# Kernel tuning notes

Measured on AMD Instinct MI355X. Metric: run time of the kernel, lower is better.

Reference implementation:

```python
import jax, jax.numpy as jnp
import numpy as np

K_NEIGHBORS = 10
SINKHORN_REG = 0.1
SINKHORN_ITERS = 50
EPS = 1e-10


def _pairwise_dist(x):
    # Euclidean cdist; clamp avoids sqrt(0) NaN grads on the diagonal
    sq = jnp.sum(x * x, axis=1)
    d2 = sq[:, None] + sq[None, :] - 2.0 * (x @ x.T)
    return jnp.sqrt(jnp.maximum(d2, 1e-12))


def setup_inputs() -> dict:
    key = jax.random.key(0)
    k1, k2 = jax.random.split(key)
    n, d = 8192, 128
    return {
        "embeddings": jax.random.normal(k1, (n, d), dtype=jnp.float32),
        "reference_embeddings": jax.random.normal(k2, (n, d), dtype=jnp.float32),
    }


def reference(embeddings, reference_embeddings):
    k = min(K_NEIGHBORS, embeddings.shape[0] - 1)

    cur_d = _pairwise_dist(embeddings)              # [n, n]
    ref_d = _pairwise_dist(reference_embeddings)    # [n, n]

    # k+1 smallest (ascending), drop self-distance column
    cur_knn = jnp.sort(cur_d, axis=1)[:, 1:k + 1]   # [n, k]
    ref_knn = jnp.sort(ref_d, axis=1)[:, 1:k + 1]   # [n, k]

    a = cur_knn / (jnp.sum(cur_knn, axis=1, keepdims=True) + EPS)  # [n, k]
    b = ref_knn / (jnp.sum(ref_knn, axis=1, keepdims=True) + EPS)  # [n, k]

    idx = jnp.arange(k, dtype=jnp.float32)
    M = jnp.abs(idx[None, :] - idx[:, None]) / k    # [k, k] shared cost
    Kmat = jnp.exp(-M / SINKHORN_REG)               # [k, k]

    # Batched Sinkhorn across all n samples at once
    def step(u, _):
        v = b / (u @ Kmat + EPS)          # K.T @ u per sample (K symmetric; explicit form u @ K)
        u = a / (v @ Kmat.T + EPS)        # K @ v per sample
        return u, None

    u0 = jnp.ones_like(a)
    u, _ = jax.lax.scan(step, u0, None, length=SINKHORN_ITERS)
    v = b / (u @ Kmat + EPS)

    # sum_ij u_i K_ij M_ij v_j per sample, then mean over n
    per_sample = jnp.einsum('ni,ij,nj->n', u, Kmat * M, v)
    return jnp.mean(per_sample)
```

## Files before the change

kernel.cpp:

```cpp
#include <hip/hip_runtime.h>
#include <hip/hip_bf16.h>
#include <math.h>

#define N 8192
#define D 128
#define NELEM (N * D)
#define KNN 10
#define EPSF 1e-10f
#define RT 32
#define NSLICE 8
#define RH 1024
#define BIGF 3.0e38f

typedef unsigned short ushort_t;
typedef short bf16x8 __attribute__((ext_vector_type(8)));
typedef float f32x4 __attribute__((ext_vector_type(4)));

template <int L>
__device__ __forceinline__ void insM(float (&l)[L], float v) {
  #pragma unroll
  for (int q = L - 1; q >= 1; --q)
    l[q] = __builtin_amdgcn_fmed3f(l[q - 1], l[q], v);
  l[0] = fminf(l[0], v);
}

__global__ void prep_kernel(const float* __restrict__ xc,
                            const float* __restrict__ xr,
                            ushort_t* __restrict__ xb,
                            ushort_t* __restrict__ xa,
                            float* __restrict__ sq) {
  int wid  = (blockIdx.x * blockDim.x + threadIdx.x) >> 6;
  int lane = threadIdx.x & 63;
  if (wid >= 2 * N) return;
  const float* x = (wid < N) ? xc : xr;
  int row = (wid < N) ? wid : wid - N;
  float2 v = *reinterpret_cast<const float2*>(x + (size_t)row * D + lane * 2);
  float s = v.x * v.x + v.y * v.y;
  #pragma unroll
  for (int off = 32; off; off >>= 1) s += __shfl_xor(s, off, 64);
  if (lane == 0) sq[wid] = s;
  auto cvt = [](float f) -> unsigned int {
    unsigned int b = __float_as_uint(f);
    return (b + 0x7FFFu + ((b >> 16) & 1u)) >> 16;
  };
  unsigned int pb = cvt(v.x) | (cvt(v.y) << 16);
  unsigned int pa = cvt(-2.f * v.x) | (cvt(-2.f * v.y) << 16);
  *reinterpret_cast<unsigned int*>(xb + (size_t)wid * D + lane * 2) = pb;
  *reinterpret_cast<unsigned int*>(xa + (size_t)wid * D + lane * 2) = pa;
}

__global__ __launch_bounds__(256, 4) void knn_mfma(
    const ushort_t* __restrict__ xb,
    const ushort_t* __restrict__ xa,
    const float* __restrict__ sq,
    float* __restrict__ partial) {
  __shared__ __align__(16) ushort_t Abuf[2][RT * D];
  __shared__ __align__(16) float SQs[RH];

  const int bid = blockIdx.x;
  const int mat = bid >> 9;
  const int colblk = (bid >> 3) & 63;
  const int slice = bid & 7;
  const ushort_t* __restrict__ XB = xb + (size_t)mat * NELEM;
  const ushort_t* __restrict__ XA = xa + (size_t)mat * NELEM;
  const float* __restrict__ SQ = sq + mat * N;
  const int r0 = slice * RH;
  const int t = threadIdx.x;
  const int w = t >> 6, l = t & 63;
  const int c0w = colblk * 128 + w * 32;

  {
    const float* gs = SQ + r0 + w * 256 + l * 4;
    float* dsts = &SQs[w * 256];
    __builtin_amdgcn_global_load_lds(
        (const __attribute__((address_space(1))) void*)gs,
        (__attribute__((address_space(3))) void*)dsts, 16, 0, 0);
  }

  bf16x8 bfr[2][4];
  #pragma unroll
  for (int j = 0; j < 2; ++j) {
    const ushort_t* p = XB + (size_t)(c0w + j * 16 + (l & 15)) * D + (l >> 4) * 8;
    #pragma unroll
    for (int kk = 0; kk < 4; ++kk)
      bfr[j][kk] = *reinterpret_cast<const bf16x8*>(p + kk * 32);
  }

  float cand[2][KNN];
  #pragma unroll
  for (int j = 0; j < 2; ++j)
    #pragma unroll
    for (int q = 0; q < KNN; ++q) cand[j][q] = BIGF;

  auto stage = [&](int tt, int bb) {
    const ushort_t* rowg = XA + (size_t)(r0 + tt * RT) * D;
    #pragma unroll
    for (int h = 0; h < 2; ++h) {
      const int rg = 2 * w + h;
      const int kk = rg >> 1, ii = rg & 1;
      const int row = ii * 16 + (l & 15);
      const int ch  = kk * 4 + (l >> 4);
      const ushort_t* g = rowg + row * D + ch * 8;
      ushort_t* dst = &Abuf[bb][rg * 512];
      __builtin_amdgcn_global_load_lds(
          (const __attribute__((address_space(1))) void*)g,
          (__attribute__((address_space(3))) void*)dst, 16, 0, 0);
    }
  };

  stage(0, 0);
  asm volatile("s_waitcnt vmcnt(0)" ::: "memory");
  __syncthreads();

  for (int tt = 0; tt < RH / RT; ++tt) {
    const int cur = tt & 1;
    if (tt < RH / RT - 1) stage(tt + 1, cur ^ 1);

    f32x4 sqi[2];
    #pragma unroll
    for (int i = 0; i < 2; ++i)
      sqi[i] = *reinterpret_cast<const f32x4*>(
          &SQs[tt * RT + i * 16 + ((l >> 4) << 2)]);

    f32x4 acc[2][2];
    #pragma unroll
    for (int i = 0; i < 2; ++i)
      #pragma unroll
      for (int j = 0; j < 2; ++j) acc[i][j] = sqi[i];

    #pragma unroll
    for (int kk = 0; kk < 4; ++kk) {
      bf16x8 af[2];
      #pragma unroll
      for (int i = 0; i < 2; ++i)
        af[i] = *reinterpret_cast<const bf16x8*>(
            &Abuf[cur][(kk * 2 + i) * 512 + l * 8]);
      #pragma unroll
      for (int i = 0; i < 2; ++i)
        #pragma unroll
        for (int j = 0; j < 2; ++j)
          acc[i][j] = __builtin_amdgcn_mfma_f32_16x16x32_bf16(af[i], bfr[j][kk],
                                                              acc[i][j], 0, 0, 0);
    }

    const int rbase = r0 + tt * RT;
    const int idiff = c0w - rbase;
    if ((unsigned)(idiff + 31) < 63u) {
      #pragma unroll
      for (int i = 0; i < 2; ++i)
        #pragma unroll
        for (int j = 0; j < 2; ++j) {
          const int dd = idiff + j * 16 + (l & 15) - i * 16 - ((l >> 4) << 2);
          #pragma unroll
          for (int r = 0; r < 4; ++r)
            if (dd == r) acc[i][j][r] = BIGF;
        }
    }

    #pragma unroll
    for (int r = 0; r < 4; ++r)
      #pragma unroll
      for (int i = 0; i < 2; ++i)
        #pragma unroll
        for (int j = 0; j < 2; ++j)
          insM<KNN>(cand[j], acc[i][j][r]);

    asm volatile("s_waitcnt vmcnt(0)" ::: "memory");
    __syncthreads();
  }

  #pragma unroll
  for (int step = 16; step <= 32; step <<= 1)
    #pragma unroll
    for (int j = 0; j < 2; ++j)
      #pragma unroll
      for (int q = 0; q < KNN; ++q) {
        float o = __shfl_xor(cand[j][q], step, 64);
        insM<KNN>(cand[j], o);
      }

  if (l < 16) {
    #pragma unroll
    for (int j = 0; j < 2; ++j) {
      const int c = c0w + j * 16 + l;
      float* dst = partial + ((size_t)(mat * N + c) * NSLICE + slice) * KNN;
      #pragma unroll
      for (int q = 0; q < KNN; ++q) dst[q] = cand[j][q];
    }
  }
}

__global__ void sink_kernel(const float* __restrict__ partial,
                            const float* __restrict__ sq,
                            float* __restrict__ ps) {
  int s = blockIdx.x * blockDim.x + threadIdx.x;
  if (s >= N) return;
  constexpr float E1 = 0.36787944117144233f;

  float a[KNN], b[KNN];
  #pragma unroll
  for (int m = 0; m < 2; ++m) {
    float best[KNN];
    #pragma unroll
    for (int q = 0; q < KNN; ++q) best[q] = BIGF;
    const float* p = partial + (size_t)(m * N + s) * NSLICE * KNN;
    for (int c = 0; c < NSLICE * KNN; ++c) insM<KNN>(best, p[c]);
    const float sqc = sq[m * N + s];
    float* dst = m ? b : a;
    #pragma unroll
    for (int q = 0; q < KNN; ++q)
      dst[q] = sqrtf(fmaxf(best[q] + sqc, 1e-12f));
  }

  float suma = 0.f, sumb = 0.f;
  #pragma unroll
  for (int q = 0; q < KNN; ++q) { suma += a[q]; sumb += b[q]; }
  float rsa = __builtin_amdgcn_rcpf(suma + EPSF);
  float rsb = __builtin_amdgcn_rcpf(sumb + EPSF);
  #pragma unroll
  for (int q = 0; q < KNN; ++q) { a[q] *= rsa; b[q] *= rsb; }

  float u_[KNN], v_[KNN];
  #pragma unroll
  for (int q = 0; q < KNN; ++q) u_[q] = 1.f;

  #pragma unroll 1
  for (int it = 0; it < 50; ++it) {
    float L[KNN], S[KNN];
    L[0] = u_[0];
    #pragma unroll
    for (int q = 1; q < KNN; ++q) L[q] = fmaf(E1, L[q - 1], u_[q]);
    S[KNN - 1] = u_[KNN - 1];
    #pragma unroll
    for (int q = KNN - 2; q >= 0; --q) S[q] = fmaf(E1, S[q + 1], u_[q]);
    #pragma unroll
    for (int q = 0; q < KNN; ++q) {
      float den = (q < KNN - 1) ? fmaf(E1, S[q + 1], L[q]) : L[KNN - 1];
      v_[q] = b[q] * __builtin_amdgcn_rcpf(den + EPSF);
    }
    L[0] = v_[0];
    #pragma unroll
    for (int q = 1; q < KNN; ++q) L[q] = fmaf(E1, L[q - 1], v_[q]);
    S[KNN - 1] = v_[KNN - 1];
    #pragma unroll
    for (int q = KNN - 2; q >= 0; --q) S[q] = fmaf(E1, S[q + 1], v_[q]);
    #pragma unroll
    for (int q = 0; q < KNN; ++q) {
      float den = (q < KNN - 1) ? fmaf(E1, S[q + 1], L[q]) : L[KNN - 1];
      u_[q] = a[q] * __builtin_amdgcn_rcpf(den + EPSF);
    }
  }
  {
    float L[KNN], S[KNN];
    L[0] = u_[0];
    #pragma unroll
    for (int q = 1; q < KNN; ++q) L[q] = fmaf(E1, L[q - 1], u_[q]);
    S[KNN - 1] = u_[KNN - 1];
    #pragma unroll
    for (int q = KNN - 2; q >= 0; --q) S[q] = fmaf(E1, S[q + 1], u_[q]);
    #pragma unroll
    for (int q = 0; q < KNN; ++q) {
      float den = (q < KNN - 1) ? fmaf(E1, S[q + 1], L[q]) : L[KNN - 1];
      v_[q] = b[q] * __builtin_amdgcn_rcpf(den + EPSF);
    }
  }
  float cost = 0.f;
  #pragma unroll
  for (int i = 0; i < KNN; ++i) {
    float accr = 0.f;
    #pragma unroll
    for (int j = 0; j < KNN; ++j) {
      const int dd = i > j ? i - j : j - i;
      const float wgt = 0.1f * (float)dd * __builtin_expf(-(float)dd);
      accr = fmaf(wgt, v_[j], accr);
    }
    cost = fmaf(u_[i], accr, cost);
  }
  ps[s] = cost;
}

__global__ void reduce_kernel(const float* __restrict__ ps, float* __restrict__ out) {
  __shared__ float red[256];
  int tid = threadIdx.x;
  float s = 0.f;
  for (int i = tid; i < N; i += 256) s += ps[i];
  red[tid] = s;
  __syncthreads();
  #pragma unroll
  for (int off = 128; off > 0; off >>= 1) {
    if (tid < off) red[tid] += red[tid + off];
    __syncthreads();
  }
  if (tid == 0) out[0] = red[0] * (1.0f / N);
}

extern "C" void kernel_launch(void* const* d_in, const int* in_sizes, int n_in,
                              void* d_out, int out_size, void* d_ws, size_t ws_size,
                              hipStream_t stream) {
  const float* xc = (const float*)d_in[0];
  const float* xr = (const float*)d_in[1];
  float* out = (float*)d_out;
  char* wsb = (char*)d_ws;

  float* sq       = (float*)wsb;
  ushort_t* xb    = (ushort_t*)(wsb + (1u << 16));
  ushort_t* xa    = (ushort_t*)(wsb + (1u << 16) + (4u << 20));
  float* partial  = (float*)(wsb + (1u << 16) + (8u << 20));
  float* ps       = partial + (size_t)2 * N * NSLICE * KNN;

  prep_kernel<<<dim3(2 * N / 4), dim3(256), 0, stream>>>(xc, xr, xb, xa, sq);
  knn_mfma<<<dim3(1024), dim3(256), 0, stream>>>(xb, xa, sq, partial);
  sink_kernel<<<dim3(N / 64), dim3(64), 0, stream>>>(partial, sq, ps);
  reduce_kernel<<<dim3(1), dim3(256), 0, stream>>>(ps, out);
}
```

Before: 115.1 us.

## Use single-wave kNN blocks loading A fragments directly from global memory

```diff
diff --git a/kernel.cpp b/kernel.cpp
--- a/kernel.cpp
+++ b/kernel.cpp
@@ -7,7 +7,7 @@
 #define NELEM (N * D)
 #define KNN 10
 #define EPSF 1e-10f
-#define RT 32
+#define RT 64
 #define NSLICE 8
 #define RH 1024
 #define BIGF 3.0e38f
@@ -49,38 +49,26 @@
   *reinterpret_cast<unsigned int*>(xa + (size_t)wid * D + lane * 2) = pa;
 }
 
-__global__ __launch_bounds__(256, 4) void knn_mfma(
+__global__ void knn_mfma(
     const ushort_t* __restrict__ xb,
     const ushort_t* __restrict__ xa,
     const float* __restrict__ sq,
     float* __restrict__ partial) {
-  __shared__ __align__(16) ushort_t Abuf[2][RT * D];
-  __shared__ __align__(16) float SQs[RH];
-
   const int bid = blockIdx.x;
-  const int mat = bid >> 9;
-  const int colblk = (bid >> 3) & 63;
+  const int mat = bid >> 11;
+  const int colgrp = (bid >> 3) & 255;
   const int slice = bid & 7;
   const ushort_t* __restrict__ XB = xb + (size_t)mat * NELEM;
   const ushort_t* __restrict__ XA = xa + (size_t)mat * NELEM;
   const float* __restrict__ SQ = sq + mat * N;
   const int r0 = slice * RH;
-  const int t = threadIdx.x;
-  const int w = t >> 6, l = t & 63;
-  const int c0w = colblk * 128 + w * 32;
-
-  {
-    const float* gs = SQ + r0 + w * 256 + l * 4;
-    float* dsts = &SQs[w * 256];
-    __builtin_amdgcn_global_load_lds(
-        (const __attribute__((address_space(1))) void*)gs,
-        (__attribute__((address_space(3))) void*)dsts, 16, 0, 0);
-  }
+  const int l = threadIdx.x;
+  const int c0 = colgrp * 32;
 
   bf16x8 bfr[2][4];
   #pragma unroll
   for (int j = 0; j < 2; ++j) {
-    const ushort_t* p = XB + (size_t)(c0w + j * 16 + (l & 15)) * D + (l >> 4) * 8;
+    const ushort_t* p = XB + (size_t)(c0 + j * 16 + (l & 15)) * D + (l >> 4) * 8;
     #pragma unroll
     for (int kk = 0; kk < 4; ++kk)
       bfr[j][kk] = *reinterpret_cast<const bf16x8*>(p + kk * 32);
@@ -92,62 +80,44 @@
     #pragma unroll
     for (int q = 0; q < KNN; ++q) cand[j][q] = BIGF;
 
-  auto stage = [&](int tt, int bb) {
-    const ushort_t* rowg = XA + (size_t)(r0 + tt * RT) * D;
-    #pragma unroll
-    for (int h = 0; h < 2; ++h) {
-      const int rg = 2 * w + h;
-      const int kk = rg >> 1, ii = rg & 1;
-      const int row = ii * 16 + (l & 15);
-      const int ch  = kk * 4 + (l >> 4);
-      const ushort_t* g = rowg + row * D + ch * 8;
-      ushort_t* dst = &Abuf[bb][rg * 512];
-      __builtin_amdgcn_global_load_lds(
-          (const __attribute__((address_space(1))) void*)g,
-          (__attribute__((address_space(3))) void*)dst, 16, 0, 0);
-    }
-  };
-
-  stage(0, 0);
-  asm volatile("s_waitcnt vmcnt(0)" ::: "memory");
-  __syncthreads();
-
   for (int tt = 0; tt < RH / RT; ++tt) {
-    const int cur = tt & 1;
-    if (tt < RH / RT - 1) stage(tt + 1, cur ^ 1);
-
-    f32x4 sqi[2];
-    #pragma unroll
-    for (int i = 0; i < 2; ++i)
+    const int rbase = r0 + tt * RT;
+
+    f32x4 sqi[4];
+    #pragma unroll
+    for (int i = 0; i < 4; ++i)
       sqi[i] = *reinterpret_cast<const f32x4*>(
-          &SQs[tt * RT + i * 16 + ((l >> 4) << 2)]);
-
-    f32x4 acc[2][2];
-    #pragma unroll
-    for (int i = 0; i < 2; ++i)
+          SQ + rbase + i * 16 + ((l >> 4) << 2));
+
+    const ushort_t* pa[4];
+    #pragma unroll
+    for (int i = 0; i < 4; ++i)
+      pa[i] = XA + (size_t)(rbase + i * 16 + (l & 15)) * D + ((l >> 4) << 3);
+
+    f32x4 acc[4][2];
+    #pragma unroll
+    for (int i = 0; i < 4; ++i)
       #pragma unroll
       for (int j = 0; j < 2; ++j) acc[i][j] = sqi[i];
 
     #pragma unroll
     for (int kk = 0; kk < 4; ++kk) {
-      bf16x8 af[2];
-      #pragma unroll
-      for (int i = 0; i < 2; ++i)
-        af[i] = *reinterpret_cast<const bf16x8*>(
-            &Abuf[cur][(kk * 2 + i) * 512 + l * 8]);
-      #pragma unroll
-      for (int i = 0; i < 2; ++i)
+      bf16x8 af[4];
+      #pragma unroll
+      for (int i = 0; i < 4; ++i)
+        af[i] = *reinterpret_cast<const bf16x8*>(pa[i] + kk * 32);
+      #pragma unroll
+      for (int i = 0; i < 4; ++i)
         #pragma unroll
         for (int j = 0; j < 2; ++j)
           acc[i][j] = __builtin_amdgcn_mfma_f32_16x16x32_bf16(af[i], bfr[j][kk],
                                                               acc[i][j], 0, 0, 0);
     }
 
-    const int rbase = r0 + tt * RT;
-    const int idiff = c0w - rbase;
-    if ((unsigned)(idiff + 31) < 63u) {
-      #pragma unroll
-      for (int i = 0; i < 2; ++i)
+    const int idiff = c0 - rbase;
+    if ((unsigned)(idiff + 31) < 95u) {
+      #pragma unroll
+      for (int i = 0; i < 4; ++i)
         #pragma unroll
         for (int j = 0; j < 2; ++j) {
           const int dd = idiff + j * 16 + (l & 15) - i * 16 - ((l >> 4) << 2);
@@ -160,13 +130,10 @@
     #pragma unroll
     for (int r = 0; r < 4; ++r)
       #pragma unroll
-      for (int i = 0; i < 2; ++i)
+      for (int i = 0; i < 4; ++i)
         #pragma unroll
         for (int j = 0; j < 2; ++j)
           insM<KNN>(cand[j], acc[i][j][r]);
-
-    asm volatile("s_waitcnt vmcnt(0)" ::: "memory");
-    __syncthreads();
   }
 
   #pragma unroll
@@ -182,7 +149,7 @@
   if (l < 16) {
     #pragma unroll
     for (int j = 0; j < 2; ++j) {
-      const int c = c0w + j * 16 + l;
+      const int c = c0 + j * 16 + l;
       float* dst = partial + ((size_t)(mat * N + c) * NSLICE + slice) * KNN;
       #pragma unroll
       for (int q = 0; q < KNN; ++q) dst[q] = cand[j][q];
@@ -309,7 +276,7 @@
   float* ps       = partial + (size_t)2 * N * NSLICE * KNN;
 
   prep_kernel<<<dim3(2 * N / 4), dim3(256), 0, stream>>>(xc, xr, xb, xa, sq);
-  knn_mfma<<<dim3(1024), dim3(256), 0, stream>>>(xb, xa, sq, partial);
-  sink_kernel<<<dim3(N / 64), dim3(64), 0, stream>>>(partial, sq, ps);
+  knn_mfma<<<dim3(4096), dim3(64), 0, stream>>>(xb, xa, sq, partial);
+  sink_kernel<<<dim3(N / 256), dim3(256), 0, stream>>>(partial, sq, ps);
   reduce_kernel<<<dim3(1), dim3(256), 0, stream>>>(ps, out);
 }
```

Result: slower. 176.0 us (+52.9%).
